# Kernel tuning notes

Hardware: AMD Instinct MI355X
Metric: run time of the kernel (lower is better)

Reference implementation:

```python
import jax, jax.numpy as jnp
import numpy as np

N_NODES = 100000
N_EDGES = 1600000
D = 128
L = 3


def setup_inputs() -> dict:
    key = jax.random.key(0)
    ks = jax.random.split(key, 5)
    x = jax.random.normal(ks[0], (N_NODES, D), dtype=jnp.float32)
    # Xavier-ish scale for stability through 3 layers
    scale = 1.0 / np.sqrt(D)
    W_self = jax.random.normal(ks[1], (L, D, D), dtype=jnp.float32) * scale
    W_neigh = jax.random.normal(ks[2], (L, D, D), dtype=jnp.float32) * scale
    bias = jnp.zeros((L, D), dtype=jnp.float32)
    src = jax.random.randint(ks[3], (N_EDGES,), 0, N_NODES)
    dst = jax.random.randint(ks[4], (N_EDGES,), 0, N_NODES)
    return {"x": x, "W_self": W_self, "W_neigh": W_neigh, "bias": bias,
            "src": src, "dst": dst}


def reference(x, W_self, W_neigh, bias, src, dst):
    """HomoSAGEEncoder forward (inference mode, dropout = identity).

    Each layer: DGL SAGEConv('mean'):
        h_neigh[v] = mean_{u in in-neighbors(v)} h[u]   (0 if no neighbors)
        h = h @ W_self + h_neigh @ W_neigh + bias
    followed by ReLU.
    """
    N = x.shape[0]
    n_layers = W_self.shape[0]
    # in-degree per destination node (shared across layers)
    deg = jax.ops.segment_sum(jnp.ones_like(dst, dtype=x.dtype), dst,
                              num_segments=N)
    inv_deg = (1.0 / jnp.maximum(deg, 1.0))[:, None]  # [N,1]

    h = x
    for l in range(n_layers):
        msg = h[src]  # [E,D] gather
        h_neigh = jax.ops.segment_sum(msg, dst, num_segments=N) * inv_deg
        h = h @ W_self[l] + h_neigh @ W_neigh[l] + bias[l]
        h = jax.nn.relu(h)
        # dropout is identity at inference; skipped
    return h
```

## Files before the change

kernel.cpp:

```cpp
#include <hip/hip_runtime.h>

typedef __attribute__((ext_vector_type(8))) short short8;
typedef __attribute__((ext_vector_type(4))) float f32x4;

static constexpr int NN = 100000;
static constexpr int NE = 1600000;
static constexpr int DD = 128;
static constexpr int NBUCK = 196;
static constexpr int CAP = 9216;

static constexpr int OFF_GCUR  = 0;
static constexpr int OFF_BBASE = 256;
static constexpr int OFF_OFFS  = 512;
static constexpr int OFF_INV   = 100516;
static constexpr int OFF_WT    = 200520;
static constexpr int OFF_SS    = 249680;
static constexpr int OFF_HB    = 1849680;
static constexpr int OFF_HNB   = 8249680;

__device__ inline ushort f2b(float f) {
  uint u = __builtin_bit_cast(uint, f);
  uint r = (u + 0x7fffu + ((u >> 16) & 1u)) >> 16;
  return (ushort)r;
}
__device__ inline float b2f(ushort b) {
  uint u = ((uint)b) << 16;
  return __builtin_bit_cast(float, u);
}

__global__ void k_zero(int* p) {
  int i = blockIdx.x * blockDim.x + threadIdx.x;
  if (i < 256) p[i] = 0;
}

__global__ void k_x2b(const float* __restrict__ x, ushort* __restrict__ hb) {
  int i = blockIdx.x * blockDim.x + threadIdx.x;
  if (i < NN * (DD / 2)) {
    float2 v = *(const float2*)(x + (size_t)i * 2);
    uint p = (uint)f2b(v.x) | ((uint)f2b(v.y) << 16);
    *(uint*)(hb + (size_t)i * 2) = p;
  }
}

__global__ void k_wt(const float* __restrict__ Ws, const float* __restrict__ Wn,
                     ushort* __restrict__ Wt) {
  int i = blockIdx.x * blockDim.x + threadIdx.x;
  if (i < 3 * 128 * 256) {
    int l = i >> 15;
    int rem = i & 32767;
    int col = rem >> 8;
    int k = rem & 255;
    float v = (k < 128) ? Ws[((size_t)l * 128 + k) * 128 + col]
                        : Wn[((size_t)l * 128 + (k - 128)) * 128 + col];
    Wt[i] = f2b(v);
  }
}

__global__ __launch_bounds__(256) void k_bucket(const int* __restrict__ src,
                                                const int* __restrict__ dst,
                                                int* __restrict__ gcur,
                                                int2* __restrict__ ebuf) {
  __shared__ int cnt[NBUCK], base[NBUCK];
  int t = threadIdx.x;
  int b0 = blockIdx.x * 4096;
  if (t < NBUCK) cnt[t] = 0;
  __syncthreads();
  int dv[16], pv[16];
#pragma unroll
  for (int j = 0; j < 16; ++j) {
    int idx = b0 + j * 256 + t;
    if (idx < NE) {
      int d = dst[idx];
      dv[j] = d;
      pv[j] = atomicAdd(&cnt[d >> 9], 1);
    } else dv[j] = -1;
  }
  __syncthreads();
  if (t < NBUCK) base[t] = atomicAdd(&gcur[t], cnt[t]);
  __syncthreads();
#pragma unroll
  for (int j = 0; j < 16; ++j) {
    if (dv[j] >= 0) {
      int idx = b0 + j * 256 + t;
      int b = dv[j] >> 9;
      int2 pr; pr.x = src[idx]; pr.y = dv[j];
      ebuf[(size_t)b * CAP + base[b] + pv[j]] = pr;
    }
  }
}

__global__ void k_bscan(const int* __restrict__ gcur, int* __restrict__ bbase) {
  __shared__ int sc[256];
  int t = threadIdx.x;
  int v = (t < NBUCK) ? gcur[t] : 0;
  sc[t] = v;
  __syncthreads();
  for (int off = 1; off < 256; off <<= 1) {
    int u = (t >= off) ? sc[t - off] : 0;
    __syncthreads();
    sc[t] += u;
    __syncthreads();
  }
  if (t < NBUCK) bbase[t] = sc[t] - v;
  if (t == 255) bbase[NBUCK] = sc[255];
}

__global__ __launch_bounds__(256) void k_sort(const int2* __restrict__ ebuf,
                                              const int* __restrict__ bbase,
                                              int* __restrict__ offs,
                                              float* __restrict__ inv,
                                              int* __restrict__ ss) {
  __shared__ int cnt[512];
  __shared__ int sbase[512];
  __shared__ int scan[256];
  __shared__ int sarr[CAP];
  int b = blockIdx.x, t = threadIdx.x;
  int base0 = bbase[b];
  int n = bbase[b + 1] - base0;
  cnt[t] = 0; cnt[t + 256] = 0;
  __syncthreads();
  const int2* eb = ebuf + (size_t)b * CAP;
  for (int i = t; i < n; i += 256) atomicAdd(&cnt[eb[i].y & 511], 1);
  __syncthreads();
  int c0 = cnt[2 * t], c1 = cnt[2 * t + 1];
  int s = c0 + c1;
  scan[t] = s;
  __syncthreads();
  for (int off = 1; off < 256; off <<= 1) {
    int u = (t >= off) ? scan[t - off] : 0;
    __syncthreads();
    scan[t] += u;
    __syncthreads();
  }
  int eb2 = scan[t] - s;
  sbase[2 * t] = eb2;
  sbase[2 * t + 1] = eb2 + c0;
  int g0 = b * 512 + 2 * t, g1 = g0 + 1;
  if (g0 < NN) {
    offs[g0] = base0 + eb2;
    inv[g0] = 1.0f / (float)(c0 > 1 ? c0 : 1);
  }
  if (g1 < NN) {
    offs[g1] = base0 + eb2 + c0;
    inv[g1] = 1.0f / (float)(c1 > 1 ? c1 : 1);
  }
  if (b == NBUCK - 1 && t == 0) offs[NN] = NE;
  cnt[2 * t] = 0; cnt[2 * t + 1] = 0;
  __syncthreads();
  for (int i = t; i < n; i += 256) {
    int2 e = eb[i];
    int ln = e.y & 511;
    int p = sbase[ln] + atomicAdd(&cnt[ln], 1);
    sarr[p] = e.x;
  }
  __syncthreads();
  for (int i = t; i < n; i += 256) ss[base0 + i] = sarr[i];
}

__global__ __launch_bounds__(256) void k_agg3(const ushort* __restrict__ h,
                                              const int* __restrict__ offs,
                                              const int* __restrict__ ss,
                                              const float* __restrict__ inv_deg,
                                              ushort* __restrict__ hN) {
  int gid = blockIdx.x * blockDim.x + threadIdx.x;
  int wid = gid >> 6;
  int lane = threadIdx.x & 63;
  int q = lane >> 4, l16 = lane & 15;
  int v = wid * 4 + q;
  int beg = offs[v], end = offs[v + 1];
  float a0 = 0, a1 = 0, a2 = 0, a3 = 0, a4 = 0, a5 = 0, a6 = 0, a7 = 0;
  const ushort* hp = h + (size_t)l16 * 8;
#define ACC8(u) { a0 += b2f((ushort)u.x); a1 += b2f((ushort)(u.x >> 16)); \
                  a2 += b2f((ushort)u.y); a3 += b2f((ushort)(u.y >> 16)); \
                  a4 += b2f((ushort)u.z); a5 += b2f((ushort)(u.z >> 16)); \
                  a6 += b2f((ushort)u.w); a7 += b2f((ushort)(u.w >> 16)); }
  int e = beg;
  for (; e + 7 < end; e += 8) {
    uint4 u0 = *(const uint4*)(hp + (size_t)ss[e + 0] * DD);
    uint4 u1 = *(const uint4*)(hp + (size_t)ss[e + 1] * DD);
    uint4 u2 = *(const uint4*)(hp + (size_t)ss[e + 2] * DD);
    uint4 u3 = *(const uint4*)(hp + (size_t)ss[e + 3] * DD);
    uint4 u4 = *(const uint4*)(hp + (size_t)ss[e + 4] * DD);
    uint4 u5 = *(const uint4*)(hp + (size_t)ss[e + 5] * DD);
    uint4 u6 = *(const uint4*)(hp + (size_t)ss[e + 6] * DD);
    uint4 u7 = *(const uint4*)(hp + (size_t)ss[e + 7] * DD);
    ACC8(u0) ACC8(u1) ACC8(u2) ACC8(u3) ACC8(u4) ACC8(u5) ACC8(u6) ACC8(u7)
  }
  for (; e < end; ++e) {
    uint4 u0 = *(const uint4*)(hp + (size_t)ss[e] * DD);
    ACC8(u0)
  }
#undef ACC8
  float w = inv_deg[v];
  a0 *= w; a1 *= w; a2 *= w; a3 *= w; a4 *= w; a5 *= w; a6 *= w; a7 *= w;
  uint4 p;
  p.x = (uint)f2b(a0) | ((uint)f2b(a1) << 16);
  p.y = (uint)f2b(a2) | ((uint)f2b(a3) << 16);
  p.z = (uint)f2b(a4) | ((uint)f2b(a5) << 16);
  p.w = (uint)f2b(a6) | ((uint)f2b(a7) << 16);
  *(uint4*)(hN + (size_t)v * DD + l16 * 8) = p;
}

__global__ __launch_bounds__(256) void k_gemm_mfma(
    const ushort* __restrict__ hA, const ushort* __restrict__ hNb,
    const ushort* __restrict__ Wt, const float* __restrict__ bias,
    ushort* __restrict__ hOutB, float* __restrict__ outF, int writeF) {
  int w = threadIdx.x >> 6;
  int lane = threadIdx.x & 63;
  int row0 = blockIdx.x * 128 + w * 32;
  int r = lane & 15;
  int kg = lane >> 4;

  f32x4 acc[2][8];
#pragma unroll
  for (int mt = 0; mt < 2; ++mt)
#pragma unroll
    for (int nt = 0; nt < 8; ++nt) acc[mt][nt] = (f32x4)0.f;

  int ra0 = row0 + r;       if (ra0 >= NN) ra0 = NN - 1;
  int ra1 = row0 + 16 + r;  if (ra1 >= NN) ra1 = NN - 1;

#pragma unroll
  for (int kt = 0; kt < 8; ++kt) {
    const ushort* hs = (kt < 4) ? hA : hNb;
    int kk = (kt & 3) * 32 + kg * 8;
    short8 a0 = *(const short8*)(hs + (size_t)ra0 * DD + kk);
    short8 a1 = *(const short8*)(hs + (size_t)ra1 * DD + kk);
    int kw = kt * 32 + kg * 8;
#pragma unroll
    for (int nt = 0; nt < 8; ++nt) {
      short8 b = *(const short8*)(Wt + (size_t)(nt * 16 + r) * 256 + kw);
      acc[0][nt] = __builtin_amdgcn_mfma_f32_16x16x32_bf16(a0, b, acc[0][nt], 0, 0, 0);
      acc[1][nt] = __builtin_amdgcn_mfma_f32_16x16x32_bf16(a1, b, acc[1][nt], 0, 0, 0);
    }
  }

  float bv[8];
#pragma unroll
  for (int nt = 0; nt < 8; ++nt) bv[nt] = bias[nt * 16 + r];

  int kg4 = kg * 4;
#pragma unroll
  for (int mt = 0; mt < 2; ++mt) {
#pragma unroll
    for (int j = 0; j < 4; ++j) {
      int row = row0 + mt * 16 + kg4 + j;
      if (row < NN) {
#pragma unroll
        for (int nt = 0; nt < 8; ++nt) {
          float val = fmaxf(acc[mt][nt][j] + bv[nt], 0.f);
          hOutB[(size_t)row * DD + nt * 16 + r] = f2b(val);
          if (writeF) outF[(size_t)row * DD + nt * 16 + r] = val;
        }
      }
    }
  }
}

extern "C" void kernel_launch(void* const* d_in, const int* in_sizes, int n_in,
                              void* d_out, int out_size, void* d_ws, size_t ws_size,
                              hipStream_t stream) {
  const float* x    = (const float*)d_in[0];
  const float* Ws   = (const float*)d_in[1];
  const float* Wn   = (const float*)d_in[2];
  const float* bias = (const float*)d_in[3];
  const int*   src  = (const int*)d_in[4];
  const int*   dst  = (const int*)d_in[5];
  float* out = (float*)d_out;

  int* ws      = (int*)d_ws;
  int* gcur    = ws + OFF_GCUR;
  int* bbase   = ws + OFF_BBASE;
  int* offs    = ws + OFF_OFFS;
  float* inv   = (float*)(ws + OFF_INV);
  ushort* Wt   = (ushort*)(ws + OFF_WT);
  int* ssorted = ws + OFF_SS;
  ushort* hB   = (ushort*)(ws + OFF_HB);
  ushort* hNb  = (ushort*)(ws + OFF_HNB);
  int2* ebuf   = (int2*)(ws + OFF_HNB);

  k_zero<<<1, 256, 0, stream>>>(gcur);
  k_x2b<<<(NN * (DD / 2) + 255) / 256, 256, 0, stream>>>(x, hB);
  k_wt<<<(3 * 128 * 256 + 255) / 256, 256, 0, stream>>>(Ws, Wn, Wt);
  k_bucket<<<(NE + 4095) / 4096, 256, 0, stream>>>(src, dst, gcur, ebuf);
  k_bscan<<<1, 256, 0, stream>>>(gcur, bbase);
  k_sort<<<NBUCK, 256, 0, stream>>>(ebuf, bbase, offs, inv, ssorted);

  for (int l = 0; l < 3; ++l) {
    k_agg3<<<NN / 4 / 4, 256, 0, stream>>>(hB, offs, ssorted, inv, hNb);
    k_gemm_mfma<<<(NN + 127) / 128, 256, 0, stream>>>(
        hB, hNb, Wt + (size_t)l * 256 * 128, bias + l * DD, hB, out, l == 2 ? 1 : 0);
  }
}
```

Baseline: 553.5 us.

## Split GEMM waves by column slice with register-resident packed weights

```diff
diff --git a/kernel.cpp b/kernel.cpp
--- a/kernel.cpp
+++ b/kernel.cpp
@@ -43,16 +43,18 @@
 }
 
 __global__ void k_wt(const float* __restrict__ Ws, const float* __restrict__ Wn,
-                     ushort* __restrict__ Wt) {
+                     ushort* __restrict__ WtP) {
   int i = blockIdx.x * blockDim.x + threadIdx.x;
-  if (i < 3 * 128 * 256) {
+  if (i < 3 * 8 * 128 * 32) {
+    int j = i & 7;
+    int kg = (i >> 3) & 3;
+    int col = (i >> 5) & 127;
+    int kt = (i >> 12) & 7;
     int l = i >> 15;
-    int rem = i & 32767;
-    int col = rem >> 8;
-    int k = rem & 255;
+    int k = kt * 32 + kg * 8 + j;
     float v = (k < 128) ? Ws[((size_t)l * 128 + k) * 128 + col]
                         : Wn[((size_t)l * 128 + (k - 128)) * 128 + col];
-    Wt[i] = f2b(v);
+    WtP[i] = f2b(v);
   }
 }
 
@@ -201,59 +203,75 @@
   *(uint4*)(hN + (size_t)v * DD + l16 * 8) = p;
 }
 
-__global__ __launch_bounds__(256) void k_gemm_mfma(
+__global__ __launch_bounds__(256) void k_gemm2(
     const ushort* __restrict__ hA, const ushort* __restrict__ hNb,
-    const ushort* __restrict__ Wt, const float* __restrict__ bias,
+    const ushort* __restrict__ WtP, const float* __restrict__ bias,
     ushort* __restrict__ hOutB, float* __restrict__ outF, int writeF) {
   int w = threadIdx.x >> 6;
   int lane = threadIdx.x & 63;
-  int row0 = blockIdx.x * 128 + w * 32;
-  int r = lane & 15;
-  int kg = lane >> 4;
-
-  f32x4 acc[2][8];
-#pragma unroll
-  for (int mt = 0; mt < 2; ++mt)
-#pragma unroll
-    for (int nt = 0; nt < 8; ++nt) acc[mt][nt] = (f32x4)0.f;
-
-  int ra0 = row0 + r;       if (ra0 >= NN) ra0 = NN - 1;
-  int ra1 = row0 + 16 + r;  if (ra1 >= NN) ra1 = NN - 1;
-
-#pragma unroll
-  for (int kt = 0; kt < 8; ++kt) {
-    const ushort* hs = (kt < 4) ? hA : hNb;
-    int kk = (kt & 3) * 32 + kg * 8;
-    short8 a0 = *(const short8*)(hs + (size_t)ra0 * DD + kk);
-    short8 a1 = *(const short8*)(hs + (size_t)ra1 * DD + kk);
-    int kw = kt * 32 + kg * 8;
-#pragma unroll
-    for (int nt = 0; nt < 8; ++nt) {
-      short8 b = *(const short8*)(Wt + (size_t)(nt * 16 + r) * 256 + kw);
-      acc[0][nt] = __builtin_amdgcn_mfma_f32_16x16x32_bf16(a0, b, acc[0][nt], 0, 0, 0);
-      acc[1][nt] = __builtin_amdgcn_mfma_f32_16x16x32_bf16(a1, b, acc[1][nt], 0, 0, 0);
+  int r = lane & 15, kg = lane >> 4;
+  int colbase = w * 32;
+
+  short8 bfrag[8][2];
+#pragma unroll
+  for (int kt = 0; kt < 8; ++kt)
+#pragma unroll
+    for (int nt = 0; nt < 2; ++nt) {
+      int col = colbase + nt * 16 + r;
+      bfrag[kt][nt] = *(const short8*)(WtP + ((size_t)(kt * 128 + col) * 4 + kg) * 8);
     }
-  }
-
-  float bv[8];
-#pragma unroll
-  for (int nt = 0; nt < 8; ++nt) bv[nt] = bias[nt * 16 + r];
-
-  int kg4 = kg * 4;
-#pragma unroll
-  for (int mt = 0; mt < 2; ++mt) {
-#pragma unroll
-    for (int j = 0; j < 4; ++j) {
-      int row = row0 + mt * 16 + kg4 + j;
-      if (row < NN) {
-#pragma unroll
-        for (int nt = 0; nt < 8; ++nt) {
-          float val = fmaxf(acc[mt][nt][j] + bv[nt], 0.f);
-          hOutB[(size_t)row * DD + nt * 16 + r] = f2b(val);
-          if (writeF) outF[(size_t)row * DD + nt * 16 + r] = val;
+
+  float bv[2];
+  bv[0] = bias[colbase + r];
+  bv[1] = bias[colbase + 16 + r];
+
+  int rowblk = blockIdx.x * 128;
+#pragma unroll 1
+  for (int half = 0; half < 2; ++half) {
+    f32x4 acc[2][2][2];
+#pragma unroll
+    for (int it = 0; it < 2; ++it) {
+      int row0 = rowblk + half * 64 + it * 32;
+      int ra0 = row0 + r;      if (ra0 > NN - 1) ra0 = NN - 1;
+      int ra1 = row0 + 16 + r; if (ra1 > NN - 1) ra1 = NN - 1;
+#pragma unroll
+      for (int mt = 0; mt < 2; ++mt)
+#pragma unroll
+        for (int nt = 0; nt < 2; ++nt) acc[it][mt][nt] = (f32x4)0.f;
+#pragma unroll
+      for (int kt = 0; kt < 8; ++kt) {
+        const ushort* hs = (kt < 4) ? hA : hNb;
+        int kk = (kt & 3) * 32 + kg * 8;
+        short8 a0 = *(const short8*)(hs + (size_t)ra0 * DD + kk);
+        short8 a1 = *(const short8*)(hs + (size_t)ra1 * DD + kk);
+        acc[it][0][0] = __builtin_amdgcn_mfma_f32_16x16x32_bf16(a0, bfrag[kt][0], acc[it][0][0], 0, 0, 0);
+        acc[it][0][1] = __builtin_amdgcn_mfma_f32_16x16x32_bf16(a0, bfrag[kt][1], acc[it][0][1], 0, 0, 0);
+        acc[it][1][0] = __builtin_amdgcn_mfma_f32_16x16x32_bf16(a1, bfrag[kt][0], acc[it][1][0], 0, 0, 0);
+        acc[it][1][1] = __builtin_amdgcn_mfma_f32_16x16x32_bf16(a1, bfrag[kt][1], acc[it][1][1], 0, 0, 0);
+      }
+    }
+    __syncthreads();
+#pragma unroll
+    for (int it = 0; it < 2; ++it) {
+      int row0 = rowblk + half * 64 + it * 32;
+#pragma unroll
+      for (int mt = 0; mt < 2; ++mt) {
+#pragma unroll
+        for (int j = 0; j < 4; ++j) {
+          int row = row0 + mt * 16 + kg * 4 + j;
+          if (row < NN) {
+#pragma unroll
+            for (int nt = 0; nt < 2; ++nt) {
+              float val = fmaxf(acc[it][mt][nt][j] + bv[nt], 0.f);
+              int col = colbase + nt * 16 + r;
+              hOutB[(size_t)row * DD + col] = f2b(val);
+              if (writeF) outF[(size_t)row * DD + col] = val;
+            }
+          }
         }
       }
     }
+    __syncthreads();
   }
 }
 
@@ -273,7 +291,7 @@
   int* bbase   = ws + OFF_BBASE;
   int* offs    = ws + OFF_OFFS;
   float* inv   = (float*)(ws + OFF_INV);
-  ushort* Wt   = (ushort*)(ws + OFF_WT);
+  ushort* WtP  = (ushort*)(ws + OFF_WT);
   int* ssorted = ws + OFF_SS;
   ushort* hB   = (ushort*)(ws + OFF_HB);
   ushort* hNb  = (ushort*)(ws + OFF_HNB);
@@ -281,14 +299,14 @@
 
   k_zero<<<1, 256, 0, stream>>>(gcur);
   k_x2b<<<(NN * (DD / 2) + 255) / 256, 256, 0, stream>>>(x, hB);
-  k_wt<<<(3 * 128 * 256 + 255) / 256, 256, 0, stream>>>(Ws, Wn, Wt);
+  k_wt<<<(3 * 8 * 128 * 32 + 255) / 256, 256, 0, stream>>>(Ws, Wn, WtP);
   k_bucket<<<(NE + 4095) / 4096, 256, 0, stream>>>(src, dst, gcur, ebuf);
   k_bscan<<<1, 256, 0, stream>>>(gcur, bbase);
   k_sort<<<NBUCK, 256, 0, stream>>>(ebuf, bbase, offs, inv, ssorted);
 
   for (int l = 0; l < 3; ++l) {
     k_agg3<<<NN / 4 / 4, 256, 0, stream>>>(hB, offs, ssorted, inv, hNb);
-    k_gemm_mfma<<<(NN + 127) / 128, 256, 0, stream>>>(
-        hB, hNb, Wt + (size_t)l * 256 * 128, bias + l * DD, hB, out, l == 2 ? 1 : 0);
-  }
-}
+    k_gemm2<<<(NN + 127) / 128, 256, 0, stream>>>(
+        hB, hNb, WtP + (size_t)l * 8 * 128 * 32, bias + l * DD, hB, out, l == 2 ? 1 : 0);
+  }
+}
```

Result: faster. 531.3 us (-4.0%).
